# Kernel optimization log

Measured on AMD Instinct MI355X. Metric: run time of the kernel, lower is better.

The kernel has to match this reference:

```python
import jax, jax.numpy as jnp
import numpy as np

SENT_LEN, SENT_BATCH, WORD_LEN = 256, 64, 16
EMB, HID = 128, 256
CEMB, CHID = 64, 128
VOCAB, CVOCAB, TAGS = 50000, 128, 50


def setup_inputs() -> dict:
    key = jax.random.key(0)
    ks = jax.random.split(key, 14)
    s = 0.1  # param init scale, avoids gate saturation
    n = lambda k, shape: (jax.random.normal(k, shape, dtype=jnp.float32) * s)
    return {
        "sentences": jax.random.randint(ks[0], (SENT_LEN, SENT_BATCH), 0, VOCAB),
        "words": jax.random.randint(ks[1], (SENT_BATCH, WORD_LEN, SENT_LEN), 0, CVOCAB),
        "char_embedding_dim": CEMB,
        "char_hidden_dim": CHID,
        "word_emb": n(ks[2], (VOCAB, EMB)),
        "char_emb": n(ks[3], (CVOCAB, CEMB)),
        "Wih_c": n(ks[4], (4 * CHID, CEMB)),
        "Whh_c": n(ks[5], (4 * CHID, CHID)),
        "bih_c": n(ks[6], (4 * CHID,)),
        "bhh_c": n(ks[7], (4 * CHID,)),
        "Wih_w": n(ks[8], (4 * HID, EMB + CHID)),
        "Whh_w": n(ks[9], (4 * HID, HID)),
        "bih_w": n(ks[10], (4 * HID,)),
        "bhh_w": n(ks[11], (4 * HID,)),
        "W_tag": n(ks[12], (TAGS, HID)),
        "b_tag": n(ks[13], (TAGS,)),
    }


def _lstm_cell(h, c, x, Wih, Whh, b):
    # torch gate order: input, forget, cell(g), output
    gates = x @ Wih.T + h @ Whh.T + b
    i, f, g, o = jnp.split(gates, 4, axis=-1)
    c_new = jax.nn.sigmoid(f) * c + jax.nn.sigmoid(i) * jnp.tanh(g)
    h_new = jax.nn.sigmoid(o) * jnp.tanh(c_new)
    return h_new, c_new


def reference(sentences, words, char_embedding_dim, char_hidden_dim,
              word_emb, char_emb, Wih_c, Whh_c, bih_c, bhh_c,
              Wih_w, Whh_w, bih_w, bhh_w, W_tag, b_tag):
    sent_len, sent_batch = sentences.shape
    dt = word_emb.dtype

    embeds = word_emb[sentences]            # [T, B, EMB]
    ce = char_emb[words]                    # [B, WL, T, CEMB]

    # char LSTM: per sentence, seq=WL, batch=T; hidden carried ACROSS sentences
    b_c = bih_c + bhh_c

    def char_sentence(carry, sent_ce):      # sent_ce: [WL, T, CEMB]
        def step(hc, x):
            h, c = _lstm_cell(hc[0], hc[1], x, Wih_c, Whh_c, b_c)
            return (h, c), None
        carry, _ = jax.lax.scan(step, carry, sent_ce)
        return carry, carry[0]               # final h: [T, CHID]

    init_c = (jnp.zeros((sent_len, CHID), dt), jnp.zeros((sent_len, CHID), dt))
    _, char_finals = jax.lax.scan(char_sentence, init_c, ce)  # [B, T, CHID]
    char_finals = jnp.transpose(char_finals, (1, 0, 2))        # [T, B, CHID]

    x = jnp.concatenate([embeds, char_finals], axis=-1)        # [T, B, EMB+CHID]

    # word LSTM over time=T, batch=B
    b_w = bih_w + bhh_w

    def word_step(hc, xt):
        h, c = _lstm_cell(hc[0], hc[1], xt, Wih_w, Whh_w, b_w)
        return (h, c), h

    init_w = (jnp.zeros((sent_batch, HID), dt), jnp.zeros((sent_batch, HID), dt))
    _, lstm_out = jax.lax.scan(word_step, init_w, x)           # [T, B, HID]

    tag_space = lstm_out @ W_tag.T + b_tag                     # [T, B, TAGS]
    return jax.nn.log_softmax(tag_space, axis=-1)
```

## Files before the change

### kernel.cpp

```cpp
#include <hip/hip_runtime.h>
#include <hip/hip_bf16.h>
#include <cstdint>

#define SENT_LEN   256
#define SENT_BATCH 64
#define WORD_LEN   16
#define EMB        128
#define HID        256
#define CEMB       64
#define CHID       128
#define TAGS       50
#define K_IN       (EMB + CHID)
#define LOG2E      1.44269504f

typedef __attribute__((ext_vector_type(8))) short short8;
typedef __attribute__((ext_vector_type(4))) float f32x4;
typedef __attribute__((ext_vector_type(4))) int   i32x4;
typedef __attribute__((ext_vector_type(2))) long  lng2;

__device__ __forceinline__ float rcpf(float x) { return __builtin_amdgcn_rcpf(x); }
__device__ __forceinline__ float sig2(float xl) {
    return rcpf(1.f + __builtin_amdgcn_exp2f(-xl));
}
__device__ __forceinline__ float tanh2(float xl) {
    xl = fminf(fmaxf(xl, -22.f), 22.f);
    float u = __builtin_amdgcn_exp2f(xl + xl);
    return (u - 1.f) * rcpf(u + 1.f);
}
__device__ __forceinline__ float lstm_act(float gi, float gf, float gg, float go, float& cst) {
    float c = sig2(gf) * cst + sig2(gi) * tanh2(gg);
    cst = c;
    return sig2(go) * tanh2(c * LOG2E);
}
__device__ __forceinline__ float bf_lo(unsigned u) { return __uint_as_float(u << 16); }
__device__ __forceinline__ float bf_hi(unsigned u) { return __uint_as_float(u & 0xffff0000u); }
__device__ __forceinline__ unsigned short f2bfu(float f) {
    unsigned u = __float_as_uint(f);
    u += 0x7fff + ((u >> 16) & 1);
    return (unsigned short)(u >> 16);
}
__device__ __forceinline__ void block_sync_lds() {
    asm volatile("s_waitcnt lgkmcnt(0)\ns_barrier" ::: "memory");
}
__device__ __forceinline__ i32x4 mfma_i8_k64(lng2 a, lng2 b, i32x4 c) {
    c = __builtin_amdgcn_mfma_i32_16x16x32_i8(a.x, b.x, c, 0, 0, 0);
    return __builtin_amdgcn_mfma_i32_16x16x32_i8(a.y, b.y, c, 0, 0, 0);
}

__global__ void prep_char(const float* __restrict__ Wih_c, const float* __restrict__ char_emb,
                          const float* __restrict__ bih_c, const float* __restrict__ bhh_c,
                          float* __restrict__ pre8) {
    int ch = blockIdx.x;
    int g  = threadIdx.x;
    float acc = bih_c[g] + bhh_c[g];
    const float* w = Wih_c + g * CEMB;
    const float* e = char_emb + ch * CEMB;
#pragma unroll
    for (int k = 0; k < CEMB; k++) acc += w[k] * e[k];
    int gt = g >> 7, j = g & 127;
    pre8[((ch * 128) + j) * 4 + gt] = acc * LOG2E;
}

__global__ void prep_wq(const float* __restrict__ Whh_w, signed char* __restrict__ wq,
                        float* __restrict__ sw) {
    int g = blockIdx.x;
    int lane = threadIdx.x;
    float4 v = reinterpret_cast<const float4*>(Whh_w + (size_t)g * HID)[lane];
    float m = fmaxf(fmaxf(fabsf(v.x), fabsf(v.y)), fmaxf(fabsf(v.z), fabsf(v.w)));
#pragma unroll
    for (int off = 32; off; off >>= 1) m = fmaxf(m, __shfl_xor(m, off, 64));
    m = fmaxf(m, 1e-20f);
    float inv = 127.f / m;
    int q0 = __float2int_rn(v.x * inv), q1 = __float2int_rn(v.y * inv);
    int q2 = __float2int_rn(v.z * inv), q3 = __float2int_rn(v.w * inv);
    int packed = (q0 & 255) | ((q1 & 255) << 8) | ((q2 & 255) << 16) | ((q3 & 255) << 24);
    reinterpret_cast<int*>(wq)[g * 64 + lane] = packed;
    if (lane == 0) sw[g] = m / 127.f;
}

__global__ __launch_bounds__(512, 1) void char_lstm(
        const int* __restrict__ words, const float* __restrict__ Whh_c,
        const float* __restrict__ pre8, float* __restrict__ cf) {
    int t    = blockIdx.x;
    int tid  = threadIdx.x;
    int lane = tid & 63, w = tid >> 6;
    int l15  = lane & 15, lq = lane >> 4;
    int j    = w * 16 + l15;

    __shared__ __align__(16) signed char hv[2][128];

    lng2 bfr[4][2];
    float swl[4];
#pragma unroll
    for (int nt = 0; nt < 4; nt++) {
        const float* wr = Whh_c + (size_t)(nt * 128 + j) * CHID;
        float v[2][16];
        float m = 0.f;
#pragma unroll
        for (int kt = 0; kt < 2; kt++) {
#pragma unroll
            for (int q = 0; q < 4; q++) {
                float4 f = reinterpret_cast<const float4*>(wr + kt * 64 + lq * 16 + q * 4)[0];
                v[kt][q * 4 + 0] = f.x; v[kt][q * 4 + 1] = f.y;
                v[kt][q * 4 + 2] = f.z; v[kt][q * 4 + 3] = f.w;
            }
#pragma unroll
            for (int p = 0; p < 16; p++) m = fmaxf(m, fabsf(v[kt][p]));
        }
        m = fmaxf(m, __shfl_xor(m, 16, 64));
        m = fmaxf(m, __shfl_xor(m, 32, 64));
        m = fmaxf(m, 1e-20f);
        float inv = 127.f / m;
#pragma unroll
        for (int kt = 0; kt < 2; kt++) {
            unsigned long lo = 0, hi = 0;
#pragma unroll
            for (int p = 0; p < 8; p++) {
                lo |= (unsigned long)((unsigned)__float2int_rn(v[kt][p] * inv) & 255) << (8 * p);
                hi |= (unsigned long)((unsigned)__float2int_rn(v[kt][p + 8] * inv) & 255) << (8 * p);
            }
            lng2 bb; bb.x = (long)lo; bb.y = (long)hi;
            bfr[nt][kt] = bb;
        }
        swl[nt] = m * (LOG2E / (127.f * 127.f));
    }
    if (tid < 64) { reinterpret_cast<int*>(hv)[tid] = 0; }

    float cst = 0.f;
    const float4* pre4p = reinterpret_cast<const float4*>(pre8);
    int cid0 = words[t];
    int cid1 = words[SENT_LEN + t];
    float4 pr0 = pre4p[cid0 * 128 + j];
    float4 pr1 = pre4p[cid1 * 128 + j];
    int cidn0 = words[2 * SENT_LEN + t];
    int cidn1 = words[3 * SENT_LEN + t];
    __syncthreads();

    for (int u = 0; u < 512; u++) {
        float4 prn0 = pre4p[cidn0 * 128 + j];
        float4 prn1 = pre4p[cidn1 * 128 + j];
        cidn0 = words[(((u << 1) + 4) & 1023) * SENT_LEN + t];
        cidn1 = words[(((u << 1) + 5) & 1023) * SENT_LEN + t];

        {
            const lng2* hp = reinterpret_cast<const lng2*>(hv[0]);
            lng2 a0 = hp[lq];
            lng2 a1 = hp[4 + lq];
            i32x4 acc[4] = {};
#pragma unroll
            for (int nt = 0; nt < 4; nt++) {
                acc[nt] = mfma_i8_k64(a0, bfr[nt][0], acc[nt]);
                acc[nt] = mfma_i8_k64(a1, bfr[nt][1], acc[nt]);
            }
            float gi = (float)acc[0][0] * swl[0] + pr0.x;
            float gf = (float)acc[1][0] * swl[1] + pr0.y;
            float gg = (float)acc[2][0] * swl[2] + pr0.z;
            float go = (float)acc[3][0] * swl[3] + pr0.w;
            float h = lstm_act(gi, gf, gg, go, cst);
            if (lq == 0)
                hv[1][j] = (signed char)__float2int_rn(h * 127.f);
            block_sync_lds();
        }
        {
            const lng2* hp = reinterpret_cast<const lng2*>(hv[1]);
            lng2 a0 = hp[lq];
            lng2 a1 = hp[4 + lq];
            i32x4 acc[4] = {};
#pragma unroll
            for (int nt = 0; nt < 4; nt++) {
                acc[nt] = mfma_i8_k64(a0, bfr[nt][0], acc[nt]);
                acc[nt] = mfma_i8_k64(a1, bfr[nt][1], acc[nt]);
            }
            float gi = (float)acc[0][0] * swl[0] + pr1.x;
            float gf = (float)acc[1][0] * swl[1] + pr1.y;
            float gg = (float)acc[2][0] * swl[2] + pr1.z;
            float go = (float)acc[3][0] * swl[3] + pr1.w;
            float h = lstm_act(gi, gf, gg, go, cst);
            if (lq == 0) {
                hv[0][j] = (signed char)__float2int_rn(h * 127.f);
                if ((u & 7) == 7)
                    cf[((size_t)t * SENT_BATCH + (u >> 3)) * CHID + j] = h;
            }
            block_sync_lds();
        }
        pr0 = prn0; pr1 = prn1;
    }
}

#define XW_SEG 65
__global__ __launch_bounds__(256, 2) void xw_gemm(
        const int* __restrict__ sentences, const float* __restrict__ word_emb,
        const float* __restrict__ cf, const float* __restrict__ Wih_w,
        const float* __restrict__ bih_w, const float* __restrict__ bhh_w,
        uint2* __restrict__ xw8) {
    __shared__ short8 Apack[32 * XW_SEG];
    __shared__ short8 Bpack[32 * XW_SEG];
    __shared__ int sid_s[64];
    int tid = threadIdx.x;
    int j0 = blockIdx.x * 16;
    int row0 = blockIdx.y * 64;
    if (tid < 64) sid_s[tid] = sentences[row0 + tid];
    __syncthreads();

#pragma unroll
    for (int it = 0; it < 8; it++) {
        int idx = it * 256 + tid;
        int m = idx >> 5, k8 = idx & 31;
        int k = k8 * 8;
        int kt = k8 >> 2, lqs = k8 & 3;
        int lanes = (m & 15) + (lqs << 4);
        int seg = kt * 4 + (m >> 4);
        const float* asrc = (k < EMB)
            ? word_emb + (size_t)sid_s[m] * EMB + k
            : cf + (size_t)(row0 + m) * CHID + (k - EMB);
        float4 a0 = reinterpret_cast<const float4*>(asrc)[0];
        float4 a1 = reinterpret_cast<const float4*>(asrc)[1];
        short8 av;
        av[0] = (short)f2bfu(a0.x); av[1] = (short)f2bfu(a0.y);
        av[2] = (short)f2bfu(a0.z); av[3] = (short)f2bfu(a0.w);
        av[4] = (short)f2bfu(a1.x); av[5] = (short)f2bfu(a1.y);
        av[6] = (short)f2bfu(a1.z); av[7] = (short)f2bfu(a1.w);
        Apack[seg * XW_SEG + lanes] = av;
        const float* bsrc = Wih_w + (size_t)((m >> 4) * 256 + j0 + (m & 15)) * K_IN + k;
        float4 b0 = reinterpret_cast<const float4*>(bsrc)[0];
        float4 b1 = reinterpret_cast<const float4*>(bsrc)[1];
        short8 bv;
        bv[0] = (short)f2bfu(b0.x); bv[1] = (short)f2bfu(b0.y);
        bv[2] = (short)f2bfu(b0.z); bv[3] = (short)f2bfu(b0.w);
        bv[4] = (short)f2bfu(b1.x); bv[5] = (short)f2bfu(b1.y);
        bv[6] = (short)f2bfu(b1.z); bv[7] = (short)f2bfu(b1.w);
        Bpack[seg * XW_SEG + lanes] = bv;
    }
    __syncthreads();

    int lane = tid & 63, wv = tid >> 6, l15 = lane & 15, lq = lane >> 4;
    f32x4 acc[4] = {{0.f,0.f,0.f,0.f},{0.f,0.f,0.f,0.f},{0.f,0.f,0.f,0.f},{0.f,0.f,0.f,0.f}};
#pragma unroll
    for (int kt = 0; kt < 8; kt++) {
        short8 a = Apack[(kt * 4 + wv) * XW_SEG + lane];
#pragma unroll
        for (int nt = 0; nt < 4; nt++)
            acc[nt] = __builtin_amdgcn_mfma_f32_16x16x32_bf16(
                a, Bpack[(kt * 4 + nt) * XW_SEG + lane], acc[nt], 0, 0, 0);
    }
    float bb[4];
#pragma unroll
    for (int nt = 0; nt < 4; nt++)
        bb[nt] = bih_w[nt * 256 + j0 + l15] + bhh_w[nt * 256 + j0 + l15];
    int t = row0 >> 6;
#pragma unroll
    for (int r = 0; r < 4; r++) {
        int b = wv * 16 + lq * 4 + r;
        uint2 o;
        o.x = (unsigned)f2bfu((acc[0][r] + bb[0]) * LOG2E)
            | ((unsigned)f2bfu((acc[1][r] + bb[1]) * LOG2E) << 16);
        o.y = (unsigned)f2bfu((acc[2][r] + bb[2]) * LOG2E)
            | ((unsigned)f2bfu((acc[3][r] + bb[3]) * LOG2E) << 16);
        xw8[((size_t)b * SENT_LEN + t) * 256 + j0 + l15] = o;
    }
}

__global__ __launch_bounds__(1024, 1) void word_lstm(
        const uint2* __restrict__ xw8, const signed char* __restrict__ wq,
        const float* __restrict__ sw, float* __restrict__ h_out) {
    int b    = blockIdx.x;
    int tid  = threadIdx.x;
    int lane = tid & 63, w = tid >> 6;
    int l15  = lane & 15, lq = lane >> 4;
    int j    = w * 16 + l15;

    __shared__ __align__(16) signed char hv[2][256];

    lng2 bfr[4][4];
    float swl[4];
#pragma unroll
    for (int nt = 0; nt < 4; nt++) {
        int g = nt * 256 + j;
        swl[nt] = sw[g] * (LOG2E / 127.f);
#pragma unroll
        for (int kt = 0; kt < 4; kt++)
            bfr[nt][kt] = reinterpret_cast<const lng2*>(wq + (size_t)g * HID + kt * 64 + lq * 16)[0];
    }
    if (tid < 128) { reinterpret_cast<int*>(hv)[tid] = 0; }

    const uint2* xwb = xw8 + (size_t)b * SENT_LEN * 256;
    float cst = 0.f;
    uint2 xq0 = xwb[0 * 256 + j];
    uint2 xq1 = xwb[1 * 256 + j];
    __syncthreads();

    for (int u = 0; u < 128; u++) {
        uint2 xn0 = xwb[((((u << 1) + 2) & 255)) * 256 + j];
        uint2 xn1 = xwb[((((u << 1) + 3) & 255)) * 256 + j];

        {
            const lng2* hp = reinterpret_cast<const lng2*>(hv[0]);
            i32x4 acc[4] = {};
#pragma unroll
            for (int kt = 0; kt < 4; kt++) {
                lng2 a = hp[kt * 4 + lq];
#pragma unroll
                for (int nt = 0; nt < 4; nt++)
                    acc[nt] = mfma_i8_k64(a, bfr[nt][kt], acc[nt]);
            }
            float gi = (float)acc[0][0] * swl[0] + bf_lo(xq0.x);
            float gf = (float)acc[1][0] * swl[1] + bf_hi(xq0.x);
            float gg = (float)acc[2][0] * swl[2] + bf_lo(xq0.y);
            float go = (float)acc[3][0] * swl[3] + bf_hi(xq0.y);
            float h = lstm_act(gi, gf, gg, go, cst);
            if (lq == 0) {
                h_out[((size_t)(u << 1) * SENT_BATCH + b) * HID + j] = h;
                hv[1][j] = (signed char)__float2int_rn(h * 127.f);
            }
            block_sync_lds();
        }
        {
            const lng2* hp = reinterpret_cast<const lng2*>(hv[1]);
            i32x4 acc[4] = {};
#pragma unroll
            for (int kt = 0; kt < 4; kt++) {
                lng2 a = hp[kt * 4 + lq];
#pragma unroll
                for (int nt = 0; nt < 4; nt++)
                    acc[nt] = mfma_i8_k64(a, bfr[nt][kt], acc[nt]);
            }
            float gi = (float)acc[0][0] * swl[0] + bf_lo(xq1.x);
            float gf = (float)acc[1][0] * swl[1] + bf_hi(xq1.x);
            float gg = (float)acc[2][0] * swl[2] + bf_lo(xq1.y);
            float go = (float)acc[3][0] * swl[3] + bf_hi(xq1.y);
            float h = lstm_act(gi, gf, gg, go, cst);
            if (lq == 0) {
                h_out[((size_t)((u << 1) + 1) * SENT_BATCH + b) * HID + j] = h;
                hv[0][j] = (signed char)__float2int_rn(h * 127.f);
            }
            block_sync_lds();
        }
        xq0 = xn0; xq1 = xn1;
    }
}

__global__ __launch_bounds__(256) void tag_logsoftmax(
        const float* __restrict__ h_out, const float* __restrict__ W_tag,
        const float* __restrict__ b_tag, float* __restrict__ out) {
    __shared__ float wt_s[TAGS * 257];
    __shared__ float hr_s[4 * HID];
    int tid = threadIdx.x;
    int row0 = blockIdx.x * 4;
#pragma unroll 2
    for (int i = 0; i < TAGS; i++) wt_s[i * 257 + tid] = W_tag[i * HID + tid];
#pragma unroll
    for (int w = 0; w < 4; w++) hr_s[w * HID + tid] = h_out[(size_t)(row0 + w) * HID + tid];
    __syncthreads();

    int w = tid >> 6, l = tid & 63;
    float acc = 0.f;
    if (l < TAGS) {
        acc = b_tag[l];
        const float* hr = hr_s + w * HID;
        const float* wr = wt_s + l * 257;
#pragma unroll 4
        for (int k = 0; k < HID; k++) acc += hr[k] * wr[k];
    }
    float m = (l < TAGS) ? acc : -1e30f;
#pragma unroll
    for (int off = 32; off; off >>= 1) m = fmaxf(m, __shfl_xor(m, off, 64));
    float e = (l < TAGS) ? __builtin_amdgcn_exp2f((acc - m) * LOG2E) : 0.f;
    float ssum = e;
#pragma unroll
    for (int off = 32; off; off >>= 1) ssum += __shfl_xor(ssum, off, 64);
    float lse = m + __logf(ssum);
    if (l < TAGS) out[(size_t)(row0 + w) * TAGS + l] = acc - lse;
}

extern "C" void kernel_launch(void* const* d_in, const int* in_sizes, int n_in,
                              void* d_out, int out_size, void* d_ws, size_t ws_size,
                              hipStream_t stream) {
    (void)in_sizes; (void)n_in; (void)out_size; (void)ws_size;
    const int*   sentences = (const int*)d_in[0];
    const int*   words     = (const int*)d_in[1];
    const float* word_emb  = (const float*)d_in[4];
    const float* char_emb  = (const float*)d_in[5];
    const float* Wih_c     = (const float*)d_in[6];
    const float* Whh_c     = (const float*)d_in[7];
    const float* bih_c     = (const float*)d_in[8];
    const float* bhh_c     = (const float*)d_in[9];
    const float* Wih_w     = (const float*)d_in[10];
    const float* Whh_w     = (const float*)d_in[11];
    const float* bih_w     = (const float*)d_in[12];
    const float* bhh_w     = (const float*)d_in[13];
    const float* W_tag     = (const float*)d_in[14];
    const float* b_tag     = (const float*)d_in[15];
    float* out = (float*)d_out;

    char* ws = (char*)d_ws;
    size_t off = 0;
    float* pre8 = (float*)(ws + off);                 off += 128 * 512 * sizeof(float);
    signed char* wq = (signed char*)(ws + off);       off += 1024 * 256;
    float* sw = (float*)(ws + off);                   off += 1024 * sizeof(float);
    off = (off + 255) & ~(size_t)255;
    float* cf = (float*)(ws + off);                   off += (size_t)SENT_LEN * SENT_BATCH * CHID * sizeof(float);
    uint2* xw8 = (uint2*)(ws + off);                  off += (size_t)SENT_LEN * SENT_BATCH * 256 * sizeof(uint2);
    float* h_out = (float*)(ws + off);                off += (size_t)SENT_LEN * SENT_BATCH * HID * sizeof(float);

    hipLaunchKernelGGL(prep_char, dim3(128), dim3(512), 0, stream,
                       Wih_c, char_emb, bih_c, bhh_c, pre8);
    hipLaunchKernelGGL(prep_wq, dim3(1024), dim3(64), 0, stream, Whh_w, wq, sw);
    hipLaunchKernelGGL(char_lstm, dim3(256), dim3(512), 0, stream,
                       words, Whh_c, pre8, cf);
    hipLaunchKernelGGL(xw_gemm, dim3(16, 256), dim3(256), 0, stream,
                       sentences, word_emb, cf, Wih_w, bih_w, bhh_w, xw8);
    hipLaunchKernelGGL(word_lstm, dim3(SENT_BATCH), dim3(1024), 0, stream,
                       xw8, wq, sw, h_out);
    hipLaunchKernelGGL(tag_logsoftmax, dim3((SENT_LEN * SENT_BATCH) / 4), dim3(256), 0, stream,
                       h_out, W_tag, b_tag, out);
}
```

Before: 1.007 ms.

## Keep Wih weights in registers across four timesteps in xw_gemm; deepen word_lstm prefetch

xw_gemm now converts each block's slice of Wih_w to bf16 fragments once, keeps them in registers, and loops over four timesteps, staging only the activation tile in LDS. Each block covers 32 hidden units, so the grid shrinks from 16x256 to 8x64 blocks. This cuts the repeated global reads and fp32-to-bf16 conversion of the weight matrix. Output columns are remapped so the word_lstm kernel can still read gate quadruples as uint2, with per-element 16-bit scattered stores. word_lstm now prefetches the input projection four steps ahead instead of two to hide load latency, at the cost of extra registers.

Result: slower. 1.045 ms (+3.8%).

```diff
diff --git a/kernel.cpp b/kernel.cpp
--- a/kernel.cpp
+++ b/kernel.cpp
@@ -187,76 +187,91 @@
     }
 }
 
-#define XW_SEG 65
+#define XA_SEG 65
 __global__ __launch_bounds__(256, 2) void xw_gemm(
         const int* __restrict__ sentences, const float* __restrict__ word_emb,
         const float* __restrict__ cf, const float* __restrict__ Wih_w,
         const float* __restrict__ bih_w, const float* __restrict__ bhh_w,
-        uint2* __restrict__ xw8) {
-    __shared__ short8 Apack[32 * XW_SEG];
-    __shared__ short8 Bpack[32 * XW_SEG];
-    __shared__ int sid_s[64];
+        unsigned short* __restrict__ xw) {
+    __shared__ short8 Apack[32 * XA_SEG];
+    __shared__ int sid_s[256];
     int tid = threadIdx.x;
-    int j0 = blockIdx.x * 16;
-    int row0 = blockIdx.y * 64;
-    if (tid < 64) sid_s[tid] = sentences[row0 + tid];
-    __syncthreads();
-
-#pragma unroll
-    for (int it = 0; it < 8; it++) {
-        int idx = it * 256 + tid;
-        int m = idx >> 5, k8 = idx & 31;
-        int k = k8 * 8;
-        int kt = k8 >> 2, lqs = k8 & 3;
-        int lanes = (m & 15) + (lqs << 4);
-        int seg = kt * 4 + (m >> 4);
-        const float* asrc = (k < EMB)
-            ? word_emb + (size_t)sid_s[m] * EMB + k
-            : cf + (size_t)(row0 + m) * CHID + (k - EMB);
-        float4 a0 = reinterpret_cast<const float4*>(asrc)[0];
-        float4 a1 = reinterpret_cast<const float4*>(asrc)[1];
-        short8 av;
-        av[0] = (short)f2bfu(a0.x); av[1] = (short)f2bfu(a0.y);
-        av[2] = (short)f2bfu(a0.z); av[3] = (short)f2bfu(a0.w);
-        av[4] = (short)f2bfu(a1.x); av[5] = (short)f2bfu(a1.y);
-        av[6] = (short)f2bfu(a1.z); av[7] = (short)f2bfu(a1.w);
-        Apack[seg * XW_SEG + lanes] = av;
-        const float* bsrc = Wih_w + (size_t)((m >> 4) * 256 + j0 + (m & 15)) * K_IN + k;
-        float4 b0 = reinterpret_cast<const float4*>(bsrc)[0];
-        float4 b1 = reinterpret_cast<const float4*>(bsrc)[1];
-        short8 bv;
-        bv[0] = (short)f2bfu(b0.x); bv[1] = (short)f2bfu(b0.y);
-        bv[2] = (short)f2bfu(b0.z); bv[3] = (short)f2bfu(b0.w);
-        bv[4] = (short)f2bfu(b1.x); bv[5] = (short)f2bfu(b1.y);
-        bv[6] = (short)f2bfu(b1.z); bv[7] = (short)f2bfu(b1.w);
-        Bpack[seg * XW_SEG + lanes] = bv;
-    }
-    __syncthreads();
-
     int lane = tid & 63, wv = tid >> 6, l15 = lane & 15, lq = lane >> 4;
-    f32x4 acc[4] = {{0.f,0.f,0.f,0.f},{0.f,0.f,0.f,0.f},{0.f,0.f,0.f,0.f},{0.f,0.f,0.f,0.f}};
-#pragma unroll
-    for (int kt = 0; kt < 8; kt++) {
-        short8 a = Apack[(kt * 4 + wv) * XW_SEG + lane];
-#pragma unroll
-        for (int nt = 0; nt < 4; nt++)
-            acc[nt] = __builtin_amdgcn_mfma_f32_16x16x32_bf16(
-                a, Bpack[(kt * 4 + nt) * XW_SEG + lane], acc[nt], 0, 0, 0);
-    }
-    float bb[4];
-#pragma unroll
-    for (int nt = 0; nt < 4; nt++)
-        bb[nt] = bih_w[nt * 256 + j0 + l15] + bhh_w[nt * 256 + j0 + l15];
-    int t = row0 >> 6;
-#pragma unroll
-    for (int r = 0; r < 4; r++) {
-        int b = wv * 16 + lq * 4 + r;
-        uint2 o;
-        o.x = (unsigned)f2bfu((acc[0][r] + bb[0]) * LOG2E)
-            | ((unsigned)f2bfu((acc[1][r] + bb[1]) * LOG2E) << 16);
-        o.y = (unsigned)f2bfu((acc[2][r] + bb[2]) * LOG2E)
-            | ((unsigned)f2bfu((acc[3][r] + bb[3]) * LOG2E) << 16);
-        xw8[((size_t)b * SENT_LEN + t) * 256 + j0 + l15] = o;
+    int j0 = blockIdx.x * 32;
+    int tg = blockIdx.y * 4;
+
+    sid_s[tid] = sentences[tg * 64 + tid];
+
+    short8 bfr[2][8];
+    float bb[2];
+#pragma unroll
+    for (int q = 0; q < 2; q++) {
+        int nt = 2 * wv + q;
+        int grow = (l15 & 3) * 256 + j0 + nt * 4 + (l15 >> 2);
+        const float* wr = Wih_w + (size_t)grow * K_IN;
+#pragma unroll
+        for (int kt = 0; kt < 8; kt++) {
+            float4 f0 = reinterpret_cast<const float4*>(wr + kt * 32 + lq * 8)[0];
+            float4 f1 = reinterpret_cast<const float4*>(wr + kt * 32 + lq * 8 + 4)[0];
+            short8 bv;
+            bv[0] = (short)f2bfu(f0.x); bv[1] = (short)f2bfu(f0.y);
+            bv[2] = (short)f2bfu(f0.z); bv[3] = (short)f2bfu(f0.w);
+            bv[4] = (short)f2bfu(f1.x); bv[5] = (short)f2bfu(f1.y);
+            bv[6] = (short)f2bfu(f1.z); bv[7] = (short)f2bfu(f1.w);
+            bfr[q][kt] = bv;
+        }
+        bb[q] = bih_w[grow] + bhh_w[grow];
+    }
+
+    for (int tt = 0; tt < 4; tt++) {
+        int t = tg + tt;
+        __syncthreads();
+#pragma unroll
+        for (int it = 0; it < 8; it++) {
+            int idx = it * 256 + tid;
+            int m = idx >> 5, k8 = idx & 31;
+            int k = k8 * 8;
+            int kt = k8 >> 2, lqs = k8 & 3;
+            const float* asrc = (k < EMB)
+                ? word_emb + (size_t)sid_s[tt * 64 + m] * EMB + k
+                : cf + (size_t)(t * 64 + m) * CHID + (k - EMB);
+            float4 a0 = reinterpret_cast<const float4*>(asrc)[0];
+            float4 a1 = reinterpret_cast<const float4*>(asrc)[1];
+            short8 av;
+            av[0] = (short)f2bfu(a0.x); av[1] = (short)f2bfu(a0.y);
+            av[2] = (short)f2bfu(a0.z); av[3] = (short)f2bfu(a0.w);
+            av[4] = (short)f2bfu(a1.x); av[5] = (short)f2bfu(a1.y);
+            av[6] = (short)f2bfu(a1.z); av[7] = (short)f2bfu(a1.w);
+            Apack[(kt * 4 + (m >> 4)) * XA_SEG + (m & 15) + (lqs << 4)] = av;
+        }
+        __syncthreads();
+
+        f32x4 acc[4][2] = {};
+#pragma unroll
+        for (int kt = 0; kt < 8; kt++) {
+#pragma unroll
+            for (int mt = 0; mt < 4; mt++) {
+                short8 a = Apack[(kt * 4 + mt) * XA_SEG + lane];
+#pragma unroll
+                for (int q = 0; q < 2; q++)
+                    acc[mt][q] = __builtin_amdgcn_mfma_f32_16x16x32_bf16(
+                        a, bfr[q][kt], acc[mt][q], 0, 0, 0);
+            }
+        }
+#pragma unroll
+        for (int q = 0; q < 2; q++) {
+            int nt = 2 * wv + q;
+            int col = (j0 + nt * 4 + (l15 >> 2)) * 4 + (l15 & 3);
+#pragma unroll
+            for (int mt = 0; mt < 4; mt++) {
+#pragma unroll
+                for (int r = 0; r < 4; r++) {
+                    int b = mt * 16 + lq * 4 + r;
+                    xw[((size_t)b * SENT_LEN + t) * 1024 + col] =
+                        f2bfu((acc[mt][q][r] + bb[q]) * LOG2E);
+                }
+            }
+        }
     }
 }
 
@@ -287,11 +302,13 @@
     float cst = 0.f;
     uint2 xq0 = xwb[0 * 256 + j];
     uint2 xq1 = xwb[1 * 256 + j];
+    uint2 xq2 = xwb[2 * 256 + j];
+    uint2 xq3 = xwb[3 * 256 + j];
     __syncthreads();
 
     for (int u = 0; u < 128; u++) {
-        uint2 xn0 = xwb[((((u << 1) + 2) & 255)) * 256 + j];
-        uint2 xn1 = xwb[((((u << 1) + 3) & 255)) * 256 + j];
+        uint2 xn0 = xwb[((((u << 1) + 4) & 255)) * 256 + j];
+        uint2 xn1 = xwb[((((u << 1) + 5) & 255)) * 256 + j];
 
         {
             const lng2* hp = reinterpret_cast<const lng2*>(hv[0]);
@@ -335,7 +352,7 @@
             }
             block_sync_lds();
         }
-        xq0 = xn0; xq1 = xn1;
+        xq0 = xq2; xq1 = xq3; xq2 = xn0; xq3 = xn1;
     }
 }
 
@@ -407,8 +424,9 @@
     hipLaunchKernelGGL(prep_wq, dim3(1024), dim3(64), 0, stream, Whh_w, wq, sw);
     hipLaunchKernelGGL(char_lstm, dim3(256), dim3(512), 0, stream,
                        words, Whh_c, pre8, cf);
-    hipLaunchKernelGGL(xw_gemm, dim3(16, 256), dim3(256), 0, stream,
-                       sentences, word_emb, cf, Wih_w, bih_w, bhh_w, xw8);
+    hipLaunchKernelGGL(xw_gemm, dim3(8, 64), dim3(256), 0, stream,
+                       sentences, word_emb, cf, Wih_w, bih_w, bhh_w,
+                       (unsigned short*)xw8);
     hipLaunchKernelGGL(word_lstm, dim3(SENT_BATCH), dim3(1024), 0, stream,
                        xw8, wq, sw, h_out);
     hipLaunchKernelGGL(tag_logsoftmax, dim3((SENT_LEN * SENT_BATCH) / 4), dim3(256), 0, stream,
```
